# Kernel tuning notes

Measured on AMD Instinct MI355X. Metric: run time of the kernel, lower is better.

## Reference

```python
import jax, jax.numpy as jnp
import numpy as np

H = 512          # hidden_size
SH = 120         # scoring_net_hidden_size
B = 1024         # batch
S = 64           # num_sentences


def setup_inputs() -> dict:
    key = jax.random.key(0)
    ks = jax.random.split(key, 12)
    sc = 0.05
    return {
        "C": jax.random.normal(ks[0], (B, S, H), jnp.float32),
        "Q": jax.random.normal(ks[1], (B, 1, H), jnp.float32),
        "prev_M": jax.random.normal(ks[2], (B, 1, H), jnp.float32),
        # scoring network params: fc1: 4H -> SH, fc2: SH -> 1
        "fc1_w": jax.random.normal(ks[3], (SH, 4 * H), jnp.float32) * sc,
        "fc1_b": jnp.zeros((SH,), jnp.float32),
        "fc2_w": jax.random.normal(ks[4], (1, SH), jnp.float32) * sc,
        "fc2_b": jnp.zeros((1,), jnp.float32),
        # GRU params (torch layout: rows ordered r, z, n)
        "W_ih": jax.random.normal(ks[5], (3 * H, H), jnp.float32) * sc,
        "W_hh": jax.random.normal(ks[6], (3 * H, H), jnp.float32) * sc,
        "b_ih": jnp.zeros((3 * H,), jnp.float32),
        "b_hh": jnp.zeros((3 * H,), jnp.float32),
    }


def reference(C, Q, prev_M, fc1_w, fc1_b, fc2_w, fc2_b, W_ih, W_hh, b_ih, b_hh):
    # --- scoring network (arch=1 feature vector) ---
    feat = jnp.concatenate(
        [C * Q, C * prev_M, jnp.abs(C - Q), jnp.abs(C - prev_M)], axis=2
    )  # [B, S, 4H]
    h1 = jnp.tanh(jnp.einsum("bsf,kf->bsk", feat, fc1_w) + fc1_b)
    G = jax.nn.sigmoid((jnp.einsum("bsk,ok->bso", h1, fc2_w) + fc2_b)[..., 0])  # [B, S]

    # --- gated GRU memory update over sentences ---
    xg_all = jnp.einsum("bsh,gh->bsg", C, W_ih) + b_ih  # [B, S, 3H] precomputed input gates

    def step(h, inp):
        xg, g = inp  # xg: [B, 3H], g: [B]
        hg = h @ W_hh.T + b_hh
        xr, xz, xn = jnp.split(xg, 3, axis=-1)
        hr, hz, hn = jnp.split(hg, 3, axis=-1)
        r = jax.nn.sigmoid(xr + hr)
        z = jax.nn.sigmoid(xz + hz)
        n = jnp.tanh(xn + r * hn)
        h_gru = (1.0 - z) * n + z * h          # standard torch GRU update
        g = g[:, None]
        h_new = g * h_gru + (1.0 - g) * h      # episodic gating
        return h_new, None

    h0 = jnp.zeros((C.shape[0], H), C.dtype)
    h_final, _ = jax.lax.scan(step, h0, (xg_all.transpose(1, 0, 2), G.T))
    return h_final[:, None, :]  # [B, 1, H]
```

## Files before the change

### kernel.cpp

```cpp
#include <hip/hip_runtime.h>
#include <hip/hip_bf16.h>

#define H_ 512
#define SH_ 120
#define B_ 1024
#define S_ 64

typedef __bf16 bf16x8 __attribute__((ext_vector_type(8)));
typedef float floatx4 __attribute__((ext_vector_type(4)));

__device__ __forceinline__ float bf2f(ushort u) {
    union { unsigned int i; float f; } v; v.i = ((unsigned int)u) << 16; return v.f;
}
__device__ __forceinline__ ushort f2bf(float f) {
    union { float f; unsigned int i; } v; v.f = f;
    unsigned int x = v.i;
    unsigned int r = (x + 0x7fffu + ((x >> 16) & 1u)) >> 16;
    return (ushort)r;
}

__global__ __launch_bounds__(256) void prep_w(
    const float* __restrict__ fc1w, ushort* __restrict__ fc1wb,
    const float* __restrict__ Wih,  ushort* __restrict__ Wihb,
    const float* __restrict__ Whh,  ushort* __restrict__ Whhb)
{
    const int stride = gridDim.x * blockDim.x;
    const int tid = blockIdx.x * blockDim.x + threadIdx.x;
    for (int i = tid; i < 61440; i += stride) {
        const float4 v = ((const float4*)fc1w)[i];
        ushort4 o; o.x = f2bf(v.x); o.y = f2bf(v.y); o.z = f2bf(v.z); o.w = f2bf(v.w);
        ((ushort4*)fc1wb)[i] = o;
    }
    for (int i = tid; i < 196608; i += stride) {
        const float4 v = ((const float4*)Wih)[i];
        ushort4 o; o.x = f2bf(v.x); o.y = f2bf(v.y); o.z = f2bf(v.z); o.w = f2bf(v.w);
        ((ushort4*)Wihb)[i] = o;
    }
    for (int i = tid; i < 196608; i += stride) {
        const float4 v = ((const float4*)Whh)[i];
        ushort4 o; o.x = f2bf(v.x); o.y = f2bf(v.y); o.z = f2bf(v.z); o.w = f2bf(v.w);
        ((ushort4*)Whhb)[i] = o;
    }
}

__global__ __launch_bounds__(256) void g_kernel(
    const float* __restrict__ C, const float* __restrict__ Q,
    const float* __restrict__ M, const ushort* __restrict__ fc1wb,
    const float* __restrict__ fc1b, const float* __restrict__ fc2w,
    const float* __restrict__ fc2b, float* __restrict__ G)
{
    __shared__ float qrow[H_];
    __shared__ float mrow[H_];
    __shared__ __align__(16) ushort featT[64 * 72];
    __shared__ __align__(16) ushort wT[128 * 72];
    __shared__ float h1s[64 * 132];

    const int b = blockIdx.x;
    const int t = threadIdx.x;
    for (int i = t; i < H_; i += 256) { qrow[i] = Q[(size_t)b * H_ + i]; mrow[i] = M[(size_t)b * H_ + i]; }

    const int wrow = t >> 1;
    const int wc0  = (t & 1) * 32;
    if (wrow >= SH_) {
        uint4* dst = (uint4*)&wT[wrow * 72 + wc0];
        const uint4 z = {0u, 0u, 0u, 0u};
        dst[0] = z; dst[1] = z; dst[2] = z; dst[3] = z;
    }
    __syncthreads();

    const int lane = t & 63;
    const int wv   = t >> 6;
    const int quad = lane >> 4;
    const int l15  = lane & 15;
    const int arow = wv * 16 + l15;
    const int s    = t >> 2;
    const int c0   = (t & 3) * 16;

    floatx4 acc[8];
#pragma unroll
    for (int i = 0; i < 8; ++i) acc[i] = (floatx4){0.f, 0.f, 0.f, 0.f};

    for (int hc = 0; hc < H_; hc += 64) {
        float cr[16];
        {
            const float4* csrc = (const float4*)(C + ((size_t)b * S_ + s) * H_ + hc + c0);
            *(float4*)&cr[0]  = csrc[0];
            *(float4*)&cr[4]  = csrc[1];
            *(float4*)&cr[8]  = csrc[2];
            *(float4*)&cr[12] = csrc[3];
        }
#pragma unroll
        for (int seg = 0; seg < 4; ++seg) {
#pragma unroll
            for (int u = 0; u < 16; ++u) {
                const int kk = c0 + u;
                const float c = cr[u];
                const float o = (seg == 0 || seg == 2) ? qrow[hc + kk] : mrow[hc + kk];
                const float v = (seg < 2) ? c * o : fabsf(c - o);
                featT[s * 72 + kk] = f2bf(v);
            }
            if (wrow < SH_) {
                const uint4* src = (const uint4*)(fc1wb + (size_t)wrow * (4 * H_) + seg * H_ + hc + wc0);
                uint4* dst = (uint4*)&wT[wrow * 72 + wc0];
                dst[0] = src[0]; dst[1] = src[1]; dst[2] = src[2]; dst[3] = src[3];
            }
            __syncthreads();
#pragma unroll
            for (int ks = 0; ks < 64; ks += 32) {
                const int ao = ks + quad * 8;
                const bf16x8 af = *(const bf16x8*)&featT[arow * 72 + ao];
#pragma unroll
                for (int nt = 0; nt < 8; ++nt) {
                    const bf16x8 bfr = *(const bf16x8*)&wT[(nt * 16 + l15) * 72 + ao];
                    acc[nt] = __builtin_amdgcn_mfma_f32_16x16x32_bf16(af, bfr, acc[nt], 0, 0, 0);
                }
            }
            __syncthreads();
        }
    }

#pragma unroll
    for (int nt = 0; nt < 8; ++nt) {
        const int col = nt * 16 + l15;
        const float bias = (col < SH_) ? fc1b[col] : 0.f;
#pragma unroll
        for (int r = 0; r < 4; ++r) {
            const int row = wv * 16 + quad * 4 + r;
            h1s[row * 132 + col] = (col < SH_) ? tanhf(acc[nt][r] + bias) : 0.f;
        }
    }
    __syncthreads();
    {
        const int part = t & 3;
        float sum = 0.f;
        for (int k = part; k < SH_; k += 4) sum += h1s[s * 132 + k] * fc2w[k];
        sum += __shfl_xor(sum, 1);
        sum += __shfl_xor(sum, 2);
        if (part == 0) {
            const float logit = sum + fc2b[0];
            G[(size_t)b * S_ + s] = 1.f / (1.f + expf(-logit));
        }
    }
}

__global__ __launch_bounds__(256) void scan_step(
    const float* __restrict__ C, const ushort* __restrict__ Wihb,
    const ushort* __restrict__ Whhb, const float* __restrict__ bih,
    const float* __restrict__ bhh, const float* __restrict__ G,
    const ushort* __restrict__ hhi_r, const ushort* __restrict__ hlo_r,
    ushort* __restrict__ hhi_w, ushort* __restrict__ hlo_w,
    float* __restrict__ out, int tstep, int last)
{
    __shared__ __align__(16) ushort As[3 * 4608];
    __shared__ __align__(16) ushort Bs[2 * 6912];

    const int bx = blockIdx.x;
    const int jt = bx & 15;
    const int bt = bx >> 4;
    const int jb = jt * 32;
    const int bb = bt * 64;
    const int t  = threadIdx.x;
    const int lane = t & 63;
    const int wv   = t >> 6;
    const int quad = lane >> 4;
    const int l15  = lane & 15;
    const int arow = wv * 16 + l15;
    const int crow = t >> 2;
    const int cc0  = (t & 3) * 16;

    floatx4 acc_r[2], acc_z[2], acc_xn[2], acc_hn[2];
#pragma unroll
    for (int i = 0; i < 2; ++i) {
        acc_r[i] = (floatx4){0.f,0.f,0.f,0.f}; acc_z[i]  = (floatx4){0.f,0.f,0.f,0.f};
        acc_xn[i]= (floatx4){0.f,0.f,0.f,0.f}; acc_hn[i] = (floatx4){0.f,0.f,0.f,0.f};
    }

    for (int kc = 0; kc < H_; kc += 64) {
        {
            const float4* src = (const float4*)(C + ((size_t)(bb + crow) * S_ + tstep) * H_ + kc + cc0);
            float cr[16];
            *(float4*)&cr[0]  = src[0];
            *(float4*)&cr[4]  = src[1];
            *(float4*)&cr[8]  = src[2];
            *(float4*)&cr[12] = src[3];
            __align__(16) ushort cb[16];
#pragma unroll
            for (int u = 0; u < 16; ++u) cb[u] = f2bf(cr[u]);
            uint4* d = (uint4*)&As[crow * 72 + cc0];
            d[0] = ((uint4*)cb)[0]; d[1] = ((uint4*)cb)[1];
        }
#pragma unroll
        for (int i = 0; i < 4; ++i) {
            const int gid  = i * 256 + t;
            const int tile = gid >> 9;
            const int rem  = gid & 511;
            const int row  = rem >> 3;
            const int grp  = rem & 7;
            const ushort* src = (tile ? hlo_r : hhi_r) + (size_t)(bb + row) * H_ + kc + grp * 8;
            *(uint4*)&As[(1 + tile) * 4608 + row * 72 + grp * 8] = *(const uint4*)src;
        }
#pragma unroll
        for (int i = 0; i < 6; ++i) {
            const int gid = i * 256 + t;
            const int mat = (gid >= 768) ? 1 : 0;
            const int rem = gid - mat * 768;
            const int row = rem >> 3;
            const int grp = rem & 7;
            const int gate = row >> 5;
            const int jj   = row & 31;
            const int grow = gate * H_ + jb + jj;
            const ushort* src = (mat ? Whhb : Wihb) + (size_t)grow * H_ + kc + grp * 8;
            *(uint4*)&Bs[mat * 6912 + row * 72 + grp * 8] = *(const uint4*)src;
        }
        __syncthreads();
#pragma unroll
        for (int ks = 0; ks < 64; ks += 32) {
            const int ao = ks + quad * 8;
            const bf16x8 a_c  = *(const bf16x8*)&As[0 * 4608 + arow * 72 + ao];
            const bf16x8 a_hh = *(const bf16x8*)&As[1 * 4608 + arow * 72 + ao];
            const bf16x8 a_hl = *(const bf16x8*)&As[2 * 4608 + arow * 72 + ao];
#pragma unroll
            for (int nt = 0; nt < 2; ++nt) {
                const int jj = nt * 16 + l15;
                const bf16x8 ih_r = *(const bf16x8*)&Bs[0 * 6912 + (0 * 32 + jj) * 72 + ao];
                const bf16x8 ih_z = *(const bf16x8*)&Bs[0 * 6912 + (1 * 32 + jj) * 72 + ao];
                const bf16x8 ih_n = *(const bf16x8*)&Bs[0 * 6912 + (2 * 32 + jj) * 72 + ao];
                const bf16x8 hh_r = *(const bf16x8*)&Bs[1 * 6912 + (0 * 32 + jj) * 72 + ao];
                const bf16x8 hh_z = *(const bf16x8*)&Bs[1 * 6912 + (1 * 32 + jj) * 72 + ao];
                const bf16x8 hh_n = *(const bf16x8*)&Bs[1 * 6912 + (2 * 32 + jj) * 72 + ao];
                acc_r[nt]  = __builtin_amdgcn_mfma_f32_16x16x32_bf16(a_c,  ih_r, acc_r[nt],  0, 0, 0);
                acc_r[nt]  = __builtin_amdgcn_mfma_f32_16x16x32_bf16(a_hh, hh_r, acc_r[nt],  0, 0, 0);
                acc_r[nt]  = __builtin_amdgcn_mfma_f32_16x16x32_bf16(a_hl, hh_r, acc_r[nt],  0, 0, 0);
                acc_z[nt]  = __builtin_amdgcn_mfma_f32_16x16x32_bf16(a_c,  ih_z, acc_z[nt],  0, 0, 0);
                acc_z[nt]  = __builtin_amdgcn_mfma_f32_16x16x32_bf16(a_hh, hh_z, acc_z[nt],  0, 0, 0);
                acc_z[nt]  = __builtin_amdgcn_mfma_f32_16x16x32_bf16(a_hl, hh_z, acc_z[nt],  0, 0, 0);
                acc_xn[nt] = __builtin_amdgcn_mfma_f32_16x16x32_bf16(a_c,  ih_n, acc_xn[nt], 0, 0, 0);
                acc_hn[nt] = __builtin_amdgcn_mfma_f32_16x16x32_bf16(a_hh, hh_n, acc_hn[nt], 0, 0, 0);
                acc_hn[nt] = __builtin_amdgcn_mfma_f32_16x16x32_bf16(a_hl, hh_n, acc_hn[nt], 0, 0, 0);
            }
        }
        __syncthreads();
    }

#pragma unroll
    for (int nt = 0; nt < 2; ++nt) {
        const int j = jb + nt * 16 + l15;
        const float br  = bih[j]          + bhh[j];
        const float bz  = bih[H_ + j]     + bhh[H_ + j];
        const float bxn = bih[2 * H_ + j];
        const float bhn = bhh[2 * H_ + j];
#pragma unroll
        for (int r4 = 0; r4 < 4; ++r4) {
            const int b = bb + wv * 16 + quad * 4 + r4;
            const size_t idx = (size_t)b * H_ + j;
            const float hold = bf2f(hhi_r[idx]) + bf2f(hlo_r[idx]);
            const float g = G[(size_t)b * S_ + tstep];
            const float rg = 1.f / (1.f + expf(-(acc_r[nt][r4] + br)));
            const float zg = 1.f / (1.f + expf(-(acc_z[nt][r4] + bz)));
            const float ng = tanhf(acc_xn[nt][r4] + bxn + rg * (acc_hn[nt][r4] + bhn));
            const float hgru = (1.f - zg) * ng + zg * hold;
            const float hnew = g * hgru + (1.f - g) * hold;
            const ushort hb = f2bf(hnew);
            hhi_w[idx] = hb;
            hlo_w[idx] = f2bf(hnew - bf2f(hb));
            if (last) out[idx] = hnew;
        }
    }
}

extern "C" void kernel_launch(void* const* d_in, const int* in_sizes, int n_in,
                              void* d_out, int out_size, void* d_ws, size_t ws_size,
                              hipStream_t stream) {
    (void)in_sizes; (void)n_in; (void)out_size; (void)ws_size;
    const float* C    = (const float*)d_in[0];
    const float* Q    = (const float*)d_in[1];
    const float* M    = (const float*)d_in[2];
    const float* fc1w = (const float*)d_in[3];
    const float* fc1b = (const float*)d_in[4];
    const float* fc2w = (const float*)d_in[5];
    const float* fc2b = (const float*)d_in[6];
    const float* Wih  = (const float*)d_in[7];
    const float* Whh  = (const float*)d_in[8];
    const float* bih  = (const float*)d_in[9];
    const float* bhh  = (const float*)d_in[10];
    float* out = (float*)d_out;

    char* ws = (char*)d_ws;
    float*  Gbuf  = (float*)ws;
    ushort* hhi0  = (ushort*)(ws + 262144);
    ushort* hlo0  = (ushort*)(ws + 262144 + 1048576);
    ushort* hhi1  = (ushort*)(ws + 262144 + 2097152);
    ushort* hlo1  = (ushort*)(ws + 262144 + 3145728);
    ushort* fc1wb = (ushort*)(ws + 4456448);
    ushort* Wihb  = (ushort*)(ws + 4947968);
    ushort* Whhb  = (ushort*)(ws + 6520832);

    hipMemsetAsync(hhi0, 0, 2097152, stream);

    prep_w<<<256, 256, 0, stream>>>(fc1w, fc1wb, Wih, Wihb, Whh, Whhb);
    g_kernel<<<B_, 256, 0, stream>>>(C, Q, M, fc1wb, fc1b, fc2w, fc2b, Gbuf);
    for (int t = 0; t < S_; ++t) {
        const ushort* hr_hi = (t & 1) ? hhi1 : hhi0;
        const ushort* hr_lo = (t & 1) ? hlo1 : hlo0;
        ushort* hw_hi = (t & 1) ? hhi0 : hhi1;
        ushort* hw_lo = (t & 1) ? hlo0 : hlo1;
        scan_step<<<256, 256, 0, stream>>>(C, Wihb, Whhb, bih, bhh, Gbuf,
                                           hr_hi, hr_lo, hw_hi, hw_lo,
                                           out, t, (t == S_ - 1) ? 1 : 0);
    }
}
```

Before: 1.459 ms.

## Fuse GRU scan into one persistent kernel with grid barrier and LDS-resident W_hh

Replaces 64 per-timestep kernel launches with a single persistent kernel of 256 blocks that synchronises between timesteps with a software grid barrier built on global atomics. Each block keeps its W_hh slice resident in LDS for all steps, prefetches the next C, W_ih and h chunks through registers while the MFMAs run, and reads the old h from LDS rather than global memory. This removes launch overhead and repeated W_hh reloads. In exchange, all 256 blocks must be co-resident or the barrier deadlocks, and the barrier counters live in device globals that are never reset by the host.

New measurement: 5.573 ms. 3.82x slower.

```diff
diff --git a/kernel.cpp b/kernel.cpp
--- a/kernel.cpp
+++ b/kernel.cpp
@@ -17,6 +17,33 @@
     unsigned int x = v.i;
     unsigned int r = (x + 0x7fffu + ((x >> 16) & 1u)) >> 16;
     return (ushort)r;
+}
+
+__device__ unsigned g_bar_cnt = 0u;
+__device__ unsigned g_bar_gen = 0u;
+
+__device__ __forceinline__ void grid_barrier_256(int tid) {
+    __threadfence();
+    __syncthreads();
+    if (tid == 0) {
+        const unsigned g = __hip_atomic_load(&g_bar_gen, __ATOMIC_RELAXED,
+                                             __HIP_MEMORY_SCOPE_AGENT);
+        const unsigned a = __hip_atomic_fetch_add(&g_bar_cnt, 1u, __ATOMIC_ACQ_REL,
+                                                  __HIP_MEMORY_SCOPE_AGENT);
+        if (a == 255u) {
+            __hip_atomic_store(&g_bar_cnt, 0u, __ATOMIC_RELAXED,
+                               __HIP_MEMORY_SCOPE_AGENT);
+            __hip_atomic_fetch_add(&g_bar_gen, 1u, __ATOMIC_RELEASE,
+                                   __HIP_MEMORY_SCOPE_AGENT);
+        } else {
+            while (__hip_atomic_load(&g_bar_gen, __ATOMIC_RELAXED,
+                                     __HIP_MEMORY_SCOPE_AGENT) == g) {
+                __builtin_amdgcn_s_sleep(2);
+            }
+        }
+    }
+    __syncthreads();
+    __threadfence();
 }
 
 __global__ __launch_bounds__(256) void prep_w(
@@ -143,20 +170,21 @@
     }
 }
 
-__global__ __launch_bounds__(256) void scan_step(
+__global__ __launch_bounds__(256) void scan_all(
     const float* __restrict__ C, const ushort* __restrict__ Wihb,
     const ushort* __restrict__ Whhb, const float* __restrict__ bih,
     const float* __restrict__ bhh, const float* __restrict__ G,
-    const ushort* __restrict__ hhi_r, const ushort* __restrict__ hlo_r,
-    ushort* __restrict__ hhi_w, ushort* __restrict__ hlo_w,
-    float* __restrict__ out, int tstep, int last)
+    ushort* __restrict__ hhi0, ushort* __restrict__ hlo0,
+    ushort* __restrict__ hhi1, ushort* __restrict__ hlo1,
+    float* __restrict__ out)
 {
-    __shared__ __align__(16) ushort As[3 * 4608];
-    __shared__ __align__(16) ushort Bs[2 * 6912];
+    __shared__ __align__(16) ushort Whh_s[96 * 520];
+    __shared__ __align__(16) ushort As[3 * 64 * 72];
+    __shared__ __align__(16) ushort Wih_s[96 * 72];
 
     const int bx = blockIdx.x;
-    const int jt = bx & 15;
-    const int bt = bx >> 4;
+    const int jt = bx >> 4;
+    const int bt = ((bx & 7) << 1) | ((bx >> 3) & 1);
     const int jb = jt * 32;
     const int bb = bt * 64;
     const int t  = threadIdx.x;
@@ -168,27 +196,52 @@
     const int crow = t >> 2;
     const int cc0  = (t & 3) * 16;
 
-    floatx4 acc_r[2], acc_z[2], acc_xn[2], acc_hn[2];
-#pragma unroll
-    for (int i = 0; i < 2; ++i) {
-        acc_r[i] = (floatx4){0.f,0.f,0.f,0.f}; acc_z[i]  = (floatx4){0.f,0.f,0.f,0.f};
-        acc_xn[i]= (floatx4){0.f,0.f,0.f,0.f}; acc_hn[i] = (floatx4){0.f,0.f,0.f,0.f};
-    }
-
-    for (int kc = 0; kc < H_; kc += 64) {
-        {
-            const float4* src = (const float4*)(C + ((size_t)(bb + crow) * S_ + tstep) * H_ + kc + cc0);
-            float cr[16];
-            *(float4*)&cr[0]  = src[0];
-            *(float4*)&cr[4]  = src[1];
-            *(float4*)&cr[8]  = src[2];
-            *(float4*)&cr[12] = src[3];
-            __align__(16) ushort cb[16];
-#pragma unroll
-            for (int u = 0; u < 16; ++u) cb[u] = f2bf(cr[u]);
-            uint4* d = (uint4*)&As[crow * 72 + cc0];
-            d[0] = ((uint4*)cb)[0]; d[1] = ((uint4*)cb)[1];
-        }
+#pragma unroll
+    for (int i = 0; i < 24; ++i) {
+        const int gid = i * 256 + t;
+        const int row = gid >> 6;
+        const int grp = gid & 63;
+        const int grow = (row >> 5) * H_ + jb + (row & 31);
+        *(uint4*)&Whh_s[row * 520 + grp * 8] =
+            *(const uint4*)(Whhb + (size_t)grow * H_ + grp * 8);
+    }
+
+    float br_[2], bz_[2], bxn_[2], bhn_[2];
+#pragma unroll
+    for (int nt = 0; nt < 2; ++nt) {
+        const int j = jb + nt * 16 + l15;
+        br_[nt]  = bih[j] + bhh[j];
+        bz_[nt]  = bih[H_ + j] + bhh[H_ + j];
+        bxn_[nt] = bih[2 * H_ + j];
+        bhn_[nt] = bhh[2 * H_ + j];
+    }
+
+    const int hold_kc  = (jb >> 6) << 6;
+    const int hold_off = jb & 63;
+
+    const ushort* hr_hi = hhi0; const ushort* hr_lo = hlo0;
+    ushort* hw_hi = hhi1; ushort* hw_lo = hlo1;
+
+    float cr[16];
+    uint4 hreg[4];
+    uint4 wreg[3];
+
+    auto load_cw = [&](int tstep, int kc) {
+        const float4* src = (const float4*)(C + ((size_t)(bb + crow) * S_ + tstep) * H_ + kc + cc0);
+        *(float4*)&cr[0]  = src[0];
+        *(float4*)&cr[4]  = src[1];
+        *(float4*)&cr[8]  = src[2];
+        *(float4*)&cr[12] = src[3];
+#pragma unroll
+        for (int i = 0; i < 3; ++i) {
+            const int gid = i * 256 + t;
+            const int row = gid >> 3;
+            const int grp = gid & 7;
+            const int grow = (row >> 5) * H_ + jb + (row & 31);
+            wreg[i] = *(const uint4*)(Wihb + (size_t)grow * H_ + kc + grp * 8);
+        }
+    };
+    auto load_h = [&](int kc) {
 #pragma unroll
         for (int i = 0; i < 4; ++i) {
             const int gid  = i * 256 + t;
@@ -196,75 +249,127 @@
             const int rem  = gid & 511;
             const int row  = rem >> 3;
             const int grp  = rem & 7;
-            const ushort* src = (tile ? hlo_r : hhi_r) + (size_t)(bb + row) * H_ + kc + grp * 8;
-            *(uint4*)&As[(1 + tile) * 4608 + row * 72 + grp * 8] = *(const uint4*)src;
-        }
-#pragma unroll
-        for (int i = 0; i < 6; ++i) {
+            const ushort* src = (tile ? hr_lo : hr_hi) + (size_t)(bb + row) * H_ + kc + grp * 8;
+            hreg[i] = *(const uint4*)src;
+        }
+    };
+    auto write_lds = [&]() {
+        __align__(16) ushort cb[16];
+#pragma unroll
+        for (int u = 0; u < 16; ++u) cb[u] = f2bf(cr[u]);
+        uint4* d = (uint4*)&As[crow * 72 + cc0];
+        d[0] = ((uint4*)cb)[0]; d[1] = ((uint4*)cb)[1];
+#pragma unroll
+        for (int i = 0; i < 4; ++i) {
+            const int gid  = i * 256 + t;
+            const int tile = gid >> 9;
+            const int rem  = gid & 511;
+            const int row  = rem >> 3;
+            const int grp  = rem & 7;
+            *(uint4*)&As[(1 + tile) * 4608 + row * 72 + grp * 8] = hreg[i];
+        }
+#pragma unroll
+        for (int i = 0; i < 3; ++i) {
             const int gid = i * 256 + t;
-            const int mat = (gid >= 768) ? 1 : 0;
-            const int rem = gid - mat * 768;
-            const int row = rem >> 3;
-            const int grp = rem & 7;
-            const int gate = row >> 5;
-            const int jj   = row & 31;
-            const int grow = gate * H_ + jb + jj;
-            const ushort* src = (mat ? Whhb : Wihb) + (size_t)grow * H_ + kc + grp * 8;
-            *(uint4*)&Bs[mat * 6912 + row * 72 + grp * 8] = *(const uint4*)src;
-        }
-        __syncthreads();
-#pragma unroll
-        for (int ks = 0; ks < 64; ks += 32) {
-            const int ao = ks + quad * 8;
-            const bf16x8 a_c  = *(const bf16x8*)&As[0 * 4608 + arow * 72 + ao];
-            const bf16x8 a_hh = *(const bf16x8*)&As[1 * 4608 + arow * 72 + ao];
-            const bf16x8 a_hl = *(const bf16x8*)&As[2 * 4608 + arow * 72 + ao];
-#pragma unroll
-            for (int nt = 0; nt < 2; ++nt) {
-                const int jj = nt * 16 + l15;
-                const bf16x8 ih_r = *(const bf16x8*)&Bs[0 * 6912 + (0 * 32 + jj) * 72 + ao];
-                const bf16x8 ih_z = *(const bf16x8*)&Bs[0 * 6912 + (1 * 32 + jj) * 72 + ao];
-                const bf16x8 ih_n = *(const bf16x8*)&Bs[0 * 6912 + (2 * 32 + jj) * 72 + ao];
-                const bf16x8 hh_r = *(const bf16x8*)&Bs[1 * 6912 + (0 * 32 + jj) * 72 + ao];
-                const bf16x8 hh_z = *(const bf16x8*)&Bs[1 * 6912 + (1 * 32 + jj) * 72 + ao];
-                const bf16x8 hh_n = *(const bf16x8*)&Bs[1 * 6912 + (2 * 32 + jj) * 72 + ao];
-                acc_r[nt]  = __builtin_amdgcn_mfma_f32_16x16x32_bf16(a_c,  ih_r, acc_r[nt],  0, 0, 0);
-                acc_r[nt]  = __builtin_amdgcn_mfma_f32_16x16x32_bf16(a_hh, hh_r, acc_r[nt],  0, 0, 0);
-                acc_r[nt]  = __builtin_amdgcn_mfma_f32_16x16x32_bf16(a_hl, hh_r, acc_r[nt],  0, 0, 0);
-                acc_z[nt]  = __builtin_amdgcn_mfma_f32_16x16x32_bf16(a_c,  ih_z, acc_z[nt],  0, 0, 0);
-                acc_z[nt]  = __builtin_amdgcn_mfma_f32_16x16x32_bf16(a_hh, hh_z, acc_z[nt],  0, 0, 0);
-                acc_z[nt]  = __builtin_amdgcn_mfma_f32_16x16x32_bf16(a_hl, hh_z, acc_z[nt],  0, 0, 0);
-                acc_xn[nt] = __builtin_amdgcn_mfma_f32_16x16x32_bf16(a_c,  ih_n, acc_xn[nt], 0, 0, 0);
-                acc_hn[nt] = __builtin_amdgcn_mfma_f32_16x16x32_bf16(a_hh, hh_n, acc_hn[nt], 0, 0, 0);
-                acc_hn[nt] = __builtin_amdgcn_mfma_f32_16x16x32_bf16(a_hl, hh_n, acc_hn[nt], 0, 0, 0);
-            }
-        }
-        __syncthreads();
-    }
-
-#pragma unroll
-    for (int nt = 0; nt < 2; ++nt) {
-        const int j = jb + nt * 16 + l15;
-        const float br  = bih[j]          + bhh[j];
-        const float bz  = bih[H_ + j]     + bhh[H_ + j];
-        const float bxn = bih[2 * H_ + j];
-        const float bhn = bhh[2 * H_ + j];
-#pragma unroll
-        for (int r4 = 0; r4 < 4; ++r4) {
-            const int b = bb + wv * 16 + quad * 4 + r4;
-            const size_t idx = (size_t)b * H_ + j;
-            const float hold = bf2f(hhi_r[idx]) + bf2f(hlo_r[idx]);
-            const float g = G[(size_t)b * S_ + tstep];
-            const float rg = 1.f / (1.f + expf(-(acc_r[nt][r4] + br)));
-            const float zg = 1.f / (1.f + expf(-(acc_z[nt][r4] + bz)));
-            const float ng = tanhf(acc_xn[nt][r4] + bxn + rg * (acc_hn[nt][r4] + bhn));
-            const float hgru = (1.f - zg) * ng + zg * hold;
-            const float hnew = g * hgru + (1.f - g) * hold;
-            const ushort hb = f2bf(hnew);
-            hhi_w[idx] = hb;
-            hlo_w[idx] = f2bf(hnew - bf2f(hb));
-            if (last) out[idx] = hnew;
-        }
+            const int row = gid >> 3;
+            const int grp = gid & 7;
+            *(uint4*)&Wih_s[row * 72 + grp * 8] = wreg[i];
+        }
+    };
+
+    load_cw(0, 0);
+    load_h(0);
+
+    for (int tstep = 0; tstep < S_; ++tstep) {
+        float g_[4];
+#pragma unroll
+        for (int r4 = 0; r4 < 4; ++r4)
+            g_[r4] = G[(size_t)(bb + wv * 16 + quad * 4 + r4) * S_ + tstep];
+
+        floatx4 acc_r[2], acc_z[2], acc_xn[2], acc_hn[2];
+#pragma unroll
+        for (int i = 0; i < 2; ++i) {
+            acc_r[i] = (floatx4){0.f,0.f,0.f,0.f}; acc_z[i]  = (floatx4){0.f,0.f,0.f,0.f};
+            acc_xn[i]= (floatx4){0.f,0.f,0.f,0.f}; acc_hn[i] = (floatx4){0.f,0.f,0.f,0.f};
+        }
+        float hold_[2][4];
+
+        for (int kc = 0; kc < H_; kc += 64) {
+            write_lds();
+            __syncthreads();
+            const int kn = kc + 64;
+            if (kn < H_) { load_cw(tstep, kn); load_h(kn); }
+            if (kc == hold_kc) {
+#pragma unroll
+                for (int nt = 0; nt < 2; ++nt)
+#pragma unroll
+                    for (int r4 = 0; r4 < 4; ++r4) {
+                        const int trow = wv * 16 + quad * 4 + r4;
+                        const int col  = hold_off + nt * 16 + l15;
+                        hold_[nt][r4] = bf2f(As[1 * 4608 + trow * 72 + col]) +
+                                        bf2f(As[2 * 4608 + trow * 72 + col]);
+                    }
+            }
+#pragma unroll
+            for (int ks = 0; ks < 64; ks += 32) {
+                const int ao = ks + quad * 8;
+                const bf16x8 a_c  = *(const bf16x8*)&As[0 * 4608 + arow * 72 + ao];
+                const bf16x8 a_hh = *(const bf16x8*)&As[1 * 4608 + arow * 72 + ao];
+                const bf16x8 a_hl = *(const bf16x8*)&As[2 * 4608 + arow * 72 + ao];
+#pragma unroll
+                for (int nt = 0; nt < 2; ++nt) {
+                    const int jj = nt * 16 + l15;
+                    const bf16x8 ih_r = *(const bf16x8*)&Wih_s[(0 * 32 + jj) * 72 + ao];
+                    const bf16x8 ih_z = *(const bf16x8*)&Wih_s[(1 * 32 + jj) * 72 + ao];
+                    const bf16x8 ih_n = *(const bf16x8*)&Wih_s[(2 * 32 + jj) * 72 + ao];
+                    const bf16x8 hh_r = *(const bf16x8*)&Whh_s[(0 * 32 + jj) * 520 + kc + ao];
+                    const bf16x8 hh_z = *(const bf16x8*)&Whh_s[(1 * 32 + jj) * 520 + kc + ao];
+                    const bf16x8 hh_n = *(const bf16x8*)&Whh_s[(2 * 32 + jj) * 520 + kc + ao];
+                    acc_r[nt]  = __builtin_amdgcn_mfma_f32_16x16x32_bf16(a_c,  ih_r, acc_r[nt],  0, 0, 0);
+                    acc_r[nt]  = __builtin_amdgcn_mfma_f32_16x16x32_bf16(a_hh, hh_r, acc_r[nt],  0, 0, 0);
+                    acc_r[nt]  = __builtin_amdgcn_mfma_f32_16x16x32_bf16(a_hl, hh_r, acc_r[nt],  0, 0, 0);
+                    acc_z[nt]  = __builtin_amdgcn_mfma_f32_16x16x32_bf16(a_c,  ih_z, acc_z[nt],  0, 0, 0);
+                    acc_z[nt]  = __builtin_amdgcn_mfma_f32_16x16x32_bf16(a_hh, hh_z, acc_z[nt],  0, 0, 0);
+                    acc_z[nt]  = __builtin_amdgcn_mfma_f32_16x16x32_bf16(a_hl, hh_z, acc_z[nt],  0, 0, 0);
+                    acc_xn[nt] = __builtin_amdgcn_mfma_f32_16x16x32_bf16(a_c,  ih_n, acc_xn[nt], 0, 0, 0);
+                    acc_hn[nt] = __builtin_amdgcn_mfma_f32_16x16x32_bf16(a_hh, hh_n, acc_hn[nt], 0, 0, 0);
+                    acc_hn[nt] = __builtin_amdgcn_mfma_f32_16x16x32_bf16(a_hl, hh_n, acc_hn[nt], 0, 0, 0);
+                }
+            }
+            __syncthreads();
+        }
+
+        const int last = (tstep == S_ - 1);
+#pragma unroll
+        for (int nt = 0; nt < 2; ++nt) {
+            const int j = jb + nt * 16 + l15;
+#pragma unroll
+            for (int r4 = 0; r4 < 4; ++r4) {
+                const int b = bb + wv * 16 + quad * 4 + r4;
+                const size_t idx = (size_t)b * H_ + j;
+                const float hold = hold_[nt][r4];
+                const float g = g_[r4];
+                const float rg = 1.f / (1.f + expf(-(acc_r[nt][r4] + br_[nt])));
+                const float zg = 1.f / (1.f + expf(-(acc_z[nt][r4] + bz_[nt])));
+                const float ng = tanhf(acc_xn[nt][r4] + bxn_[nt] + rg * (acc_hn[nt][r4] + bhn_[nt]));
+                const float hgru = (1.f - zg) * ng + zg * hold;
+                const float hnew = g * hgru + (1.f - g) * hold;
+                const ushort hb = f2bf(hnew);
+                hw_hi[idx] = hb;
+                hw_lo[idx] = f2bf(hnew - bf2f(hb));
+                if (last) out[idx] = hnew;
+            }
+        }
+        if (last) break;
+
+        {
+            const ushort* th = hr_hi; const ushort* tl = hr_lo;
+            hr_hi = (const ushort*)hw_hi; hr_lo = (const ushort*)hw_lo;
+            hw_hi = (ushort*)th; hw_lo = (ushort*)tl;
+        }
+        load_cw(tstep + 1, 0);
+        grid_barrier_256(t);
+        load_h(0);
     }
 }
 
@@ -299,13 +404,6 @@
 
     prep_w<<<256, 256, 0, stream>>>(fc1w, fc1wb, Wih, Wihb, Whh, Whhb);
     g_kernel<<<B_, 256, 0, stream>>>(C, Q, M, fc1wb, fc1b, fc2w, fc2b, Gbuf);
-    for (int t = 0; t < S_; ++t) {
-        const ushort* hr_hi = (t & 1) ? hhi1 : hhi0;
-        const ushort* hr_lo = (t & 1) ? hlo1 : hlo0;
-        ushort* hw_hi = (t & 1) ? hhi0 : hhi1;
-        ushort* hw_lo = (t & 1) ? hlo0 : hlo1;
-        scan_step<<<256, 256, 0, stream>>>(C, Wihb, Whhb, bih, bhh, Gbuf,
-                                           hr_hi, hr_lo, hw_hi, hw_lo,
-                                           out, t, (t == S_ - 1) ? 1 : 0);
-    }
-}
+    scan_all<<<256, 256, 0, stream>>>(C, Wihb, Whhb, bih, bhh, Gbuf,
+                                      hhi0, hlo0, hhi1, hlo1, out);
+}
```
